# Performance work log

Measured on AMD Instinct MI355X. Metric: run time of the kernel, lower is better.

## Reference

```python
import jax, jax.numpy as jnp
import numpy as np

T, B, N, GH, GW, ENC, H, D, TH = 16, 512, 8192, 3, 13, 128, 4, 32, 64
G = GH * GW          # 39 social grid cells
EMB = H * D          # 128 = n_head * att_out
SCALE = 1.0 / np.sqrt(ENC).astype(np.float32)
LN_EPS = 1e-5


def lstm(x, Wih, Whh, bih, bhh):
    # x: [T, Batch, in] -> hidden states [T, Batch, ENC]; torch gate order i,f,g,o
    n = x.shape[1]
    h0 = jnp.zeros((n, ENC), x.dtype)

    def step(carry, xt):
        h, c = carry
        g = xt @ Wih.T + bih + h @ Whh.T + bhh
        i, f, gg, o = jnp.split(g, 4, axis=-1)
        c = jax.nn.sigmoid(f) * c + jax.nn.sigmoid(i) * jnp.tanh(gg)
        h = jax.nn.sigmoid(o) * jnp.tanh(c)
        return (h, c), h

    _, hs = jax.lax.scan(step, (h0, h0), x)
    return hs


def glu(x, Wa, ba, Wg, bg):
    return (x @ Wa.T + ba) * jax.nn.sigmoid(x @ Wg.T + bg)


def layer_norm(x, g, b):
    m = jnp.mean(x, -1, keepdims=True)
    v = jnp.var(x, -1, keepdims=True)
    return (x - m) * jax.lax.rsqrt(v + LN_EPS) * g + b


def setup_inputs():
    key = jax.random.key(0)
    ks = jax.random.split(key, 40)

    def rn(i, sh, s=1.0):
        return jax.random.normal(ks[i], sh, jnp.float32) * s

    inp = {
        'hist': rn(0, (T, B, 2)), 'nbrs': rn(1, (T, N, 2)),
        'va': rn(2, (T, B, 2)), 'nbrsva': rn(3, (T, N, 2)),
        'lane': jnp.zeros((T, B, 1), jnp.float32),
        'nbrslane': jnp.zeros((T, N, 1), jnp.float32),
        'cls': rn(4, (T, B, 1)), 'nbrscls': rn(5, (T, N, 1)),
    }
    # boolean social-grid mask with exactly N true cells (cell-level, full enc dim)
    rng = np.random.default_rng(0)
    flat = np.zeros(B * G, bool)
    flat[rng.permutation(B * G)[:N]] = True
    inp['mask'] = jnp.asarray(np.broadcast_to(flat.reshape(B, GH, GW, 1), (B, GH, GW, ENC)))

    s = 0.05
    inp.update({
        'W1': rn(6, (TH, 5), s), 'b1': jnp.zeros((TH,), jnp.float32),
        'Wih': rn(7, (4 * ENC, TH), s), 'Whh': rn(8, (4 * ENC, ENC), s),
        'bih': jnp.zeros((4 * ENC,), jnp.float32), 'bhh': jnp.zeros((4 * ENC,), jnp.float32),
        'Wq': rn(9, (EMB, ENC), s), 'bq': jnp.zeros((EMB,), jnp.float32),
        'Wk': rn(10, (EMB, ENC), s), 'bk': jnp.zeros((EMB,), jnp.float32),
        'Wv': rn(11, (EMB, ENC), s), 'bv': jnp.zeros((EMB,), jnp.float32),
        'Wg1a': rn(12, (ENC, EMB), s), 'bg1a': jnp.zeros((ENC,), jnp.float32),
        'Wg1g': rn(13, (ENC, EMB), s), 'bg1g': jnp.zeros((ENC,), jnp.float32),
        'Wqt': rn(14, (EMB, ENC), s), 'bqt': jnp.zeros((EMB,), jnp.float32),
        'Wkt': rn(15, (EMB, ENC), s), 'bkt': jnp.zeros((EMB,), jnp.float32),
        'Wvt': rn(16, (EMB, ENC), s), 'bvt': jnp.zeros((EMB,), jnp.float32),
        'Wg2a': rn(17, (ENC, EMB), s), 'bg2a': jnp.zeros((ENC,), jnp.float32),
        'Wg2g': rn(18, (ENC, EMB), s), 'bg2g': jnp.zeros((ENC,), jnp.float32),
        'ln_g': jnp.ones((ENC,), jnp.float32), 'ln_b': jnp.zeros((ENC,), jnp.float32),
    })
    return inp


def reference(hist, nbrs, mask, va, nbrsva, lane, nbrslane, cls, nbrscls,
              W1, b1, Wih, Whh, bih, bhh, Wq, bq, Wk, bk, Wv, bv,
              Wg1a, bg1a, Wg1g, bg1g, Wqt, bqt, Wkt, bkt, Wvt, bvt,
              Wg2a, bg2a, Wg2g, bg2g, ln_g, ln_b):
    # f_length == 5 branch
    hist_in = jnp.concatenate((hist, cls, va), -1)        # [T,B,5]
    nbrs_in = jnp.concatenate((nbrs, nbrscls, nbrsva), -1)  # [T,N,5]

    hist_enc = jax.nn.elu(hist_in @ W1.T + b1)
    hist_h = lstm(hist_enc, Wih, Whh, bih, bhh)           # [T,B,ENC]
    hist_hidden = jnp.transpose(hist_h, (1, 0, 2))        # [B,T,ENC]

    nbrs_enc = jax.nn.elu(nbrs_in @ W1.T + b1)
    nbrs_h = lstm(nbrs_enc, Wih, Whh, bih, bhh)           # [T,N,ENC]

    # masked_scatter: fill true grid cells (row-major over B*G) with neighbor states
    cell = mask[:, :, :, 0].reshape(B * G)                # [B*G] bool
    idx = jnp.cumsum(cell.astype(jnp.int32)) - 1          # position among true cells
    gathered = nbrs_h[:, jnp.clip(idx, 0, N - 1), :]      # [T,B*G,ENC]
    soc = jnp.where(cell[None, :, None], gathered, 0.0).reshape(T, B, G, ENC)

    # spatial multi-head attention (each timestep attends over its own grid)
    q = (hist_hidden @ Wq.T + bq).reshape(B, T, H, D)
    k = (soc @ Wk.T + bk).reshape(T, B, G, H, D)
    v = (soc @ Wv.T + bv).reshape(T, B, G, H, D)
    a = jax.nn.softmax(jnp.einsum('bthd,tbghd->bthg', q, k) * SCALE, -1)
    spa = jnp.einsum('bthg,tbghd->bthd', a, v).reshape(B, T, EMB)
    spa = glu(spa, Wg1a, bg1a, Wg1g, bg1g)

    values = layer_norm(hist_hidden + spa, ln_g, ln_b)    # [B,T,ENC]

    # temporal multi-head attention over T
    qt = (values @ Wqt.T + bqt).reshape(B, T, H, D)
    kt = (values @ Wkt.T + bkt).reshape(B, T, H, D)
    vt = (values @ Wvt.T + bvt).reshape(B, T, H, D)
    at = jax.nn.softmax(jnp.einsum('bthd,bshd->bhts', qt, kt) * SCALE, -1)
    tmp = jnp.einsum('bhts,bshd->bthd', at, vt).reshape(B, T, EMB)
    tmp = glu(tmp, Wg2a, bg2a, Wg2g, bg2g)

    # use_spatial=True
    return layer_norm(hist_hidden + spa + tmp, ln_g, ln_b)
```

## Files before the change

kernel.cpp:

```cpp
#include <hip/hip_runtime.h>
#include <math.h>

#define T_ 16
#define B_ 512
#define N_ 8192
#define G_ 39
#define ENC_ 128
#define TH_ 64
#define MROWS 8704
#define GATE 512
#define KCAT 192
#define SCALE_ 0.08838834764831845f
#define LNEPS 1e-5f
#define NBLK 136

typedef short bf16x8 __attribute__((ext_vector_type(8)));
typedef float f32x4  __attribute__((ext_vector_type(4)));

__device__ __forceinline__ float sigm(float x){ return 1.0f/(1.0f+expf(-x)); }
__device__ __forceinline__ float rcpf(float x){ return __builtin_amdgcn_rcpf(x); }
__device__ __forceinline__ float sigm_f(float x){ return rcpf(1.0f + __expf(-x)); }
__device__ __forceinline__ float tanh_f(float x){ return 1.0f - 2.0f*rcpf(__expf(2.0f*x) + 1.0f); }
__device__ __forceinline__ unsigned short f2bf(float f){
  unsigned int u = __float_as_uint(f);
  unsigned int r = u + 0x7FFFu + ((u>>16)&1u);
  return (unsigned short)(r>>16);
}
__device__ __forceinline__ float bf2f(unsigned short h){
  return __uint_as_float(((unsigned int)h)<<16);
}

__global__ __launch_bounds__(256) void k_prep(
    const float* __restrict__ Wih, const float* __restrict__ Whh,
    const float* __restrict__ bih, const float* __restrict__ bhh,
    const float* __restrict__ Wk,  const float* __restrict__ Wv,
    const float* __restrict__ Wq,
    const float* __restrict__ Wqt, const float* __restrict__ bqt,
    const float* __restrict__ Wkt, const float* __restrict__ bkt,
    const float* __restrict__ Wvt, const float* __restrict__ bvt,
    const float* __restrict__ Wg1a, const float* __restrict__ bg1a,
    const float* __restrict__ Wg1g, const float* __restrict__ bg1g,
    const float* __restrict__ Wg2a, const float* __restrict__ bg2a,
    const float* __restrict__ Wg2g, const float* __restrict__ bg2g,
    unsigned short* __restrict__ WcatB, float* __restrict__ biasg,
    unsigned short* __restrict__ WqB,
    unsigned short* __restrict__ WkD,  unsigned short* __restrict__ WvD,
    float* __restrict__ zero512,
    unsigned short* __restrict__ WqktB, float* __restrict__ bqkt,
    unsigned short* __restrict__ Wg1B,  float* __restrict__ bg1,
    unsigned short* __restrict__ Wg2B,  float* __restrict__ bg2)
{
  int i = blockIdx.x*256 + threadIdx.x;
  if (i < GATE*KCAT) {
    int n = i / KCAT, k = i % KCAT;
    WcatB[i] = f2bf((k < TH_) ? Wih[n*TH_ + k] : Whh[n*ENC_ + (k - TH_)]);
  }
  if (i < GATE) biasg[i] = bih[i] + bhh[i];
  if (i < ENC_*ENC_) WqB[i] = f2bf(Wq[i]);
  if (i < 512*128) {
    int r = i >> 7, dc = i & 127;
    int h = r >> 7, e = r & 127;
    WkD[i] = ((dc >> 5) == h) ? f2bf(Wk[dc*128 + e]) : (unsigned short)0;
  }
  if (i < 128*512) {
    int r = i >> 9, kk = i & 511;
    int hp = kk >> 7, e = kk & 127;
    WvD[i] = (hp == (r >> 5)) ? f2bf(Wv[r*128 + e]) : (unsigned short)0;
  }
  if (i < 512) zero512[i] = 0.0f;
  if (i < 2*ENC_*ENC_) {
    int n = i >> 7, k = i & 127;
    Wg1B[i] = f2bf((n < ENC_) ? Wg1a[n*ENC_ + k] : Wg1g[(n-ENC_)*ENC_ + k]);
    Wg2B[i] = f2bf((n < ENC_) ? Wg2a[n*ENC_ + k] : Wg2g[(n-ENC_)*ENC_ + k]);
  }
  if (i < 2*ENC_) {
    bg1[i] = (i < ENC_) ? bg1a[i] : bg1g[i-ENC_];
    bg2[i] = (i < ENC_) ? bg2a[i] : bg2g[i-ENC_];
  }
  if (i < 3*ENC_*ENC_) {
    int n = i >> 7, k = i & 127;
    float w = (n < ENC_) ? Wqt[n*ENC_ + k] : (n < 2*ENC_) ? Wkt[(n-ENC_)*ENC_ + k]
                                                          : Wvt[(n-2*ENC_)*ENC_ + k];
    WqktB[i] = f2bf(w);
  }
  if (i < 3*ENC_) bqkt[i] = (i < ENC_) ? bqt[i] : (i < 2*ENC_) ? bkt[i-ENC_] : bvt[i-2*ENC_];
}

__device__ __forceinline__ int cellval(const unsigned char* m, long cell, int w) {
  long byte = cell * 128L * w;
  if (w == 1) return m[byte] != 0;
  if (w == 2) return *(const unsigned short*)(m + byte) != 0;
  if (w == 4) return *(const unsigned int*)(m + byte) != 0;
  return *(const unsigned long long*)(m + byte) != 0ULL;
}
__device__ __forceinline__ int cellconsist(const unsigned char* m, long cell, int w) {
  long byte = cell * 128L * w;
  if (w == 1) { unsigned char v = m[byte];
    for (int j = 1; j < 8; ++j) if (m[byte + j] != v) return 0; return 1; }
  if (w == 2) { unsigned short v = *(const unsigned short*)(m + byte);
    for (int j = 1; j < 8; ++j) if (*(const unsigned short*)(m + byte + 2L*j) != v) return 0; return 1; }
  if (w == 4) { unsigned int v = *(const unsigned int*)(m + byte);
    for (int j = 1; j < 8; ++j) if (*(const unsigned int*)(m + byte + 4L*j) != v) return 0; return 1; }
  unsigned long long v = *(const unsigned long long*)(m + byte);
  for (int j = 1; j < 8; ++j) if (*(const unsigned long long*)(m + byte + 8L*j) != v) return 0; return 1;
}

__global__ void k_detect(const unsigned char* __restrict__ mask, int* __restrict__ wsel)
{
  __shared__ int bad;
  int tid = threadIdx.x;
  int chosen = 0;
  for (int w = 1; w <= 8 && !chosen; w <<= 1) {
    if (tid == 0) bad = 0;
    __syncthreads();
    int ok = 1;
    for (int c = tid; c < 512; c += 256) ok &= cellconsist(mask, c, w);
    if (!ok) bad = 1;
    __syncthreads();
    if (!bad) chosen = w;
    __syncthreads();
  }
  if (tid == 0) *wsel = chosen ? chosen : 1;
}

__global__ void k_count(const unsigned char* __restrict__ mask,
                        const int* __restrict__ wsel, int* __restrict__ bcnt)
{
  __shared__ int sc[256];
  int tid = threadIdx.x;
  long cell = (long)blockIdx.x*256 + tid;
  sc[tid] = cellval(mask, cell, *wsel);
  __syncthreads();
  for (int off = 128; off; off >>= 1) {
    if (tid < off) sc[tid] += sc[tid + off];
    __syncthreads();
  }
  if (tid == 0) bcnt[blockIdx.x] = sc[0];
}

__global__ void k_fill(const unsigned char* __restrict__ mask,
                       const int* __restrict__ wsel, const int* __restrict__ bcnt,
                       int* __restrict__ nidx)
{
  __shared__ int sc[256];
  int tid = threadIdx.x, blk = blockIdx.x;
  long cell = (long)blk*256 + tid;
  int on = cellval(mask, cell, *wsel);
  sc[tid] = on;
  __syncthreads();
  for (int off = 1; off < 256; off <<= 1) {
    int v = (tid >= off) ? sc[tid - off] : 0;
    __syncthreads();
    sc[tid] += v;
    __syncthreads();
  }
  int base = 0;
  for (int i = 0; i < blk; ++i) base += bcnt[i];
  nidx[cell] = on ? (base + sc[tid] - 1) : -1;
}

__global__ __launch_bounds__(256) void k_encode_all(
    const float* __restrict__ hist, const float* __restrict__ cls, const float* __restrict__ va,
    const float* __restrict__ nbrs, const float* __restrict__ nbrscls, const float* __restrict__ nbrsva,
    const float* __restrict__ W1, const float* __restrict__ b1,
    unsigned short* __restrict__ XencB)
{
  int i = blockIdx.x*256 + threadIdx.x;
  int t = blockIdx.y;
  int o = i & 63, m = i >> 6;
  float in0, in1, in2, in3, in4;
  if (m < B_) {
    int r = t*B_ + m;
    in0 = hist[r*2]; in1 = hist[r*2+1]; in2 = cls[r]; in3 = va[r*2]; in4 = va[r*2+1];
  } else {
    int r = t*N_ + (m - B_);
    in0 = nbrs[r*2]; in1 = nbrs[r*2+1]; in2 = nbrscls[r]; in3 = nbrsva[r*2]; in4 = nbrsva[r*2+1];
  }
  const float* w = W1 + o*5;
  float s = b1[o] + in0*w[0] + in1*w[1] + in2*w[2] + in3*w[3] + in4*w[4];
  XencB[((long)t*MROWS + m)*64 + o] = f2bf((s > 0.0f) ? s : expm1f(s));
}

struct AP {
  const unsigned short *Xenc, *Wcat, *Wq;
  const float *biasg, *bq;
  float *hh;
  unsigned short *qB;
  unsigned short *HnB;
};

__global__ __launch_bounds__(512, 1) void k_lstm(AP p)
{
  __shared__ unsigned short Hl[2*64*128];

  const int tid = threadIdx.x;
  const int w = tid >> 6, l = tid & 63;
  const int lr = l & 15, lk = (l >> 4) * 8, lq = (l >> 4) * 4;
  const int bi = blockIdx.x, bm = bi * 64;
  const bool ish = (bi < 8);

  bf16x8 wgx[4][2], wgh[4][4];
  #pragma unroll
  for (int g = 0; g < 4; ++g) {
    #pragma unroll
    for (int ks = 0; ks < 2; ++ks)
      wgx[g][ks] = *(const bf16x8*)(p.Wcat + (long)(g*128 + w*16 + lr)*KCAT + ks*32 + lk);
    #pragma unroll
    for (int ks = 0; ks < 4; ++ks)
      wgh[g][ks] = *(const bf16x8*)(p.Wcat + (long)(g*128 + w*16 + lr)*KCAT + 64 + ks*32 + lk);
  }

  const int ch = w*16 + lr;
  float bgv[4];
  #pragma unroll
  for (int g = 0; g < 4; ++g) bgv[g] = p.biasg[g*128 + ch];
  const float bqv = ish ? p.bq[ch] : 0.0f;

  for (int i = tid; i < 64*128; i += 512) Hl[i] = 0;
  float creg[4][4];
  #pragma unroll
  for (int mi = 0; mi < 4; ++mi)
    #pragma unroll
    for (int q = 0; q < 4; ++q) creg[mi][q] = 0.0f;

  bf16x8 axc[2][4];
  #pragma unroll
  for (int ks = 0; ks < 2; ++ks)
    #pragma unroll
    for (int mi = 0; mi < 4; ++mi)
      axc[ks][mi] = *(const bf16x8*)(p.Xenc + ((long)0*MROWS + bm + mi*16 + lr)*64 + ks*32 + lk);

  __syncthreads();

  int cur = 0;
  for (int t = 0; t < T_; ++t) {
    f32x4 acc[4][4];
    #pragma unroll
    for (int g = 0; g < 4; ++g)
      #pragma unroll
      for (int mi = 0; mi < 4; ++mi) {
        f32x4 v = { bgv[g], bgv[g], bgv[g], bgv[g] };
        acc[g][mi] = v;
      }
    #pragma unroll
    for (int ks = 0; ks < 2; ++ks)
      #pragma unroll
      for (int g = 0; g < 4; ++g)
        #pragma unroll
        for (int mi = 0; mi < 4; ++mi)
          acc[g][mi] = __builtin_amdgcn_mfma_f32_16x16x32_bf16(axc[ks][mi], wgx[g][ks], acc[g][mi], 0, 0, 0);
    if (t + 1 < T_) {
      #pragma unroll
      for (int ks = 0; ks < 2; ++ks)
        #pragma unroll
        for (int mi = 0; mi < 4; ++mi)
          axc[ks][mi] = *(const bf16x8*)(p.Xenc + ((long)(t+1)*MROWS + bm + mi*16 + lr)*64 + ks*32 + lk);
    }
    #pragma unroll
    for (int ks = 0; ks < 4; ++ks) {
      bf16x8 a[4];
      #pragma unroll
      for (int mi = 0; mi < 4; ++mi) {
        int row = mi*16 + lr;
        int col = (ks*32 + lk) ^ ((row & 7) << 3);
        a[mi] = *(const bf16x8*)(Hl + cur*8192 + row*128 + col);
      }
      #pragma unroll
      for (int g = 0; g < 4; ++g)
        #pragma unroll
        for (int mi = 0; mi < 4; ++mi)
          acc[g][mi] = __builtin_amdgcn_mfma_f32_16x16x32_bf16(a[mi], wgh[g][ks], acc[g][mi], 0, 0, 0);
    }
    int nxt = cur ^ 1;
    #pragma unroll
    for (int mi = 0; mi < 4; ++mi)
      #pragma unroll
      for (int q = 0; q < 4; ++q) {
        int row = mi*16 + lq + q;
        float gi = acc[0][mi][q];
        float gf = acc[1][mi][q];
        float gg = acc[2][mi][q];
        float go = acc[3][mi][q];
        float cc = sigm_f(gf)*creg[mi][q] + sigm_f(gi)*tanh_f(gg);
        creg[mi][q] = cc;
        float hv = sigm_f(go)*tanh_f(cc);
        Hl[nxt*8192 + row*128 + (ch ^ ((row & 7) << 3))] = f2bf(hv);
        if (ish) p.hh[((long)(bm + row)*T_ + t)*128 + ch] = hv;
      }
    __builtin_amdgcn_sched_barrier(0);
    asm volatile("s_waitcnt lgkmcnt(0)" ::: "memory");
    __builtin_amdgcn_s_barrier();
    __builtin_amdgcn_sched_barrier(0);
    cur = nxt;
    if (ish) {
      f32x4 a2[4];
      #pragma unroll
      for (int mi = 0; mi < 4; ++mi) {
        f32x4 v = { bqv, bqv, bqv, bqv };
        a2[mi] = v;
      }
      #pragma unroll
      for (int ks = 0; ks < 4; ++ks) {
        bf16x8 b = *(const bf16x8*)(p.Wq + (long)(w*16 + lr)*128 + ks*32 + lk);
        #pragma unroll
        for (int mi = 0; mi < 4; ++mi) {
          int row = mi*16 + lr;
          int col = (ks*32 + lk) ^ ((row & 7) << 3);
          bf16x8 a = *(const bf16x8*)(Hl + cur*8192 + row*128 + col);
          a2[mi] = __builtin_amdgcn_mfma_f32_16x16x32_bf16(a, b, a2[mi], 0, 0, 0);
        }
      }
      #pragma unroll
      for (int mi = 0; mi < 4; ++mi)
        #pragma unroll
        for (int q = 0; q < 4; ++q)
          p.qB[((long)t*B_ + bm + mi*16 + lq + q)*128 + ch] = f2bf(a2[mi][q]);
    } else {
      for (int e = tid; e < 64*16; e += 512) {
        int r = e >> 4, j = e & 15;
        int src = cur*8192 + r*128 + ((j*8) ^ ((r & 7) << 3));
        *(bf16x8*)(p.HnB + ((long)t*N_ + (bm - B_) + r)*128 + j*8) =
            *(const bf16x8*)(Hl + src);
      }
    }
  }
}

__global__ __launch_bounds__(128) void k_attn2(
    const unsigned short* __restrict__ qB,
    const unsigned short* __restrict__ qWB,
    const unsigned short* __restrict__ HnB,
    const float* __restrict__ bk,
    const int* __restrict__ nidx,
    unsigned short* __restrict__ hbarB)
{
  __shared__ int sn[G_];
  __shared__ unsigned short hL[G_*128];
  __shared__ float sgh[G_][4];
  int blk = blockIdx.x;
  int b = blk >> 4, t = blk & 15;
  int tid = threadIdx.x;
  int h = tid >> 5, d = tid & 31;
  if (tid < G_) sn[tid] = nidx[b*G_ + tid];
  __syncthreads();
  for (int g = 0; g < G_; ++g) {
    int ni = sn[g];
    if (ni >= 0) hL[g*128 + tid] = HnB[((long)t*N_ + ni)*128 + tid];
  }
  float qel = bf2f(qB[((long)t*B_ + b)*128 + tid]);
  float qbk = qel * bk[tid];
  #pragma unroll
  for (int off = 16; off; off >>= 1) qbk += __shfl_xor(qbk, off);
  float qw[4];
  #pragma unroll
  for (int j = 0; j < 4; ++j)
    qw[j] = bf2f(qWB[((long)t*B_ + b)*512 + h*128 + d + j*32]);
  __syncthreads();
  for (int g = 0; g < G_; ++g) {
    float s;
    if (sn[g] >= 0) {
      float part = 0.0f;
      #pragma unroll
      for (int j = 0; j < 4; ++j) part += bf2f(hL[g*128 + d + j*32]) * qw[j];
      #pragma unroll
      for (int off = 16; off; off >>= 1) part += __shfl_xor(part, off);
      s = (part + qbk) * SCALE_;
    } else {
      s = qbk * SCALE_;
    }
    if (d == 0) sgh[g][h] = s;
  }
  float mx = -1e30f;
  for (int g = 0; g < G_; ++g) mx = fmaxf(mx, sgh[g][h]);
  float den = 0.0f;
  float hb[4] = {0.0f, 0.0f, 0.0f, 0.0f};
  for (int g = 0; g < G_; ++g) {
    float e = expf(sgh[g][h] - mx);
    den += e;
    if (sn[g] >= 0) {
      #pragma unroll
      for (int j = 0; j < 4; ++j) hb[j] += e * bf2f(hL[g*128 + d + j*32]);
    }
  }
  float inv = 1.0f / den;
  #pragma unroll
  for (int j = 0; j < 4; ++j)
    hbarB[((long)b*T_ + t)*512 + h*128 + d + j*32] = f2bf(hb[j] * inv);
}

__global__ __launch_bounds__(256) void k_gemm_bf16(
    const unsigned short* __restrict__ A, int lda,
    const unsigned short* __restrict__ W, int ldw,
    const float* __restrict__ bias,
    float* __restrict__ C, int ldc, int K)
{
  int tid = threadIdx.x;
  int w = tid >> 6, l = tid & 63;
  int lr = l & 15, lk = (l >> 4) * 8, lq = (l >> 4) * 4;
  int bm = blockIdx.x * 64;
  int bn = blockIdx.y * 128 + w * 32;
  f32x4 acc[4][2] = {};
  for (int k0 = 0; k0 < K; k0 += 32) {
    bf16x8 a[4], b[2];
    #pragma unroll
    for (int mi = 0; mi < 4; ++mi)
      a[mi] = *(const bf16x8*)(A + (long)(bm + mi*16 + lr)*lda + k0 + lk);
    #pragma unroll
    for (int ni = 0; ni < 2; ++ni)
      b[ni] = *(const bf16x8*)(W + (long)(bn + ni*16 + lr)*ldw + k0 + lk);
    #pragma unroll
    for (int mi = 0; mi < 4; ++mi)
      #pragma unroll
      for (int ni = 0; ni < 2; ++ni)
        acc[mi][ni] = __builtin_amdgcn_mfma_f32_16x16x32_bf16(a[mi], b[ni], acc[mi][ni], 0, 0, 0);
  }
  #pragma unroll
  for (int mi = 0; mi < 4; ++mi)
    #pragma unroll
    for (int ni = 0; ni < 2; ++ni) {
      int col = bn + ni*16 + lr;
      float bb = bias[col];
      #pragma unroll
      for (int q = 0; q < 4; ++q)
        C[(long)(bm + mi*16 + lq + q)*ldc + col] = acc[mi][ni][q] + bb;
    }
}

__global__ __launch_bounds__(256) void k_gemm_bf16o(
    const unsigned short* __restrict__ A, int lda,
    const unsigned short* __restrict__ W, int ldw,
    const float* __restrict__ bias,
    unsigned short* __restrict__ C, int ldc, int K)
{
  int tid = threadIdx.x;
  int w = tid >> 6, l = tid & 63;
  int lr = l & 15, lk = (l >> 4) * 8, lq = (l >> 4) * 4;
  int bm = blockIdx.x * 64;
  int bn = blockIdx.y * 128 + w * 32;
  f32x4 acc[4][2] = {};
  for (int k0 = 0; k0 < K; k0 += 32) {
    bf16x8 a[4], b[2];
    #pragma unroll
    for (int mi = 0; mi < 4; ++mi)
      a[mi] = *(const bf16x8*)(A + (long)(bm + mi*16 + lr)*lda + k0 + lk);
    #pragma unroll
    for (int ni = 0; ni < 2; ++ni)
      b[ni] = *(const bf16x8*)(W + (long)(bn + ni*16 + lr)*ldw + k0 + lk);
    #pragma unroll
    for (int mi = 0; mi < 4; ++mi)
      #pragma unroll
      for (int ni = 0; ni < 2; ++ni)
        acc[mi][ni] = __builtin_amdgcn_mfma_f32_16x16x32_bf16(a[mi], b[ni], acc[mi][ni], 0, 0, 0);
  }
  #pragma unroll
  for (int mi = 0; mi < 4; ++mi)
    #pragma unroll
    for (int ni = 0; ni < 2; ++ni) {
      int col = bn + ni*16 + lr;
      float bb = bias[col];
      #pragma unroll
      for (int q = 0; q < 4; ++q)
        C[(long)(bm + mi*16 + lq + q)*ldc + col] = f2bf(acc[mi][ni][q] + bb);
    }
}

__global__ __launch_bounds__(256) void k_glu_addln(
    const float* __restrict__ t12, const float* __restrict__ res,
    const float* __restrict__ lg, const float* __restrict__ lb,
    float* __restrict__ sum_out, unsigned short* __restrict__ ln_bf16,
    float* __restrict__ ln_f32)
{
  int gtid = blockIdx.x*256 + threadIdx.x;
  int r = gtid >> 6;
  int l = threadIdx.x & 63;
  if (r >= B_*T_) return;
  long b4 = (long)r*256, b2 = (long)r*128;
  float xA = res[b2 + l]      + t12[b4 + l]      * sigm(t12[b4 + 128 + l]);
  float xB = res[b2 + 64 + l] + t12[b4 + 64 + l] * sigm(t12[b4 + 192 + l]);
  if (sum_out) { sum_out[b2 + l] = xA; sum_out[b2 + 64 + l] = xB; }
  float s = xA + xB, s2 = xA*xA + xB*xB;
  #pragma unroll
  for (int off = 32; off; off >>= 1) { s += __shfl_xor(s, off); s2 += __shfl_xor(s2, off); }
  float mean = s * (1.0f/128.0f);
  float var  = s2 * (1.0f/128.0f) - mean*mean;
  float inv  = rsqrtf(var + LNEPS);
  float oA = (xA - mean)*inv*lg[l]      + lb[l];
  float oB = (xB - mean)*inv*lg[64 + l] + lb[64 + l];
  if (ln_bf16) { ln_bf16[b2 + l] = f2bf(oA); ln_bf16[b2 + 64 + l] = f2bf(oB); }
  if (ln_f32)  { ln_f32[b2 + l] = oA;        ln_f32[b2 + 64 + l] = oB; }
}

__global__ __launch_bounds__(128) void k_attn_t(
    const unsigned short* __restrict__ qkt, unsigned short* __restrict__ out)
{
  int b = blockIdx.x, tid = threadIdx.x;
  __shared__ float sq[16][128], sk[16][128], sv[16][128];
  __shared__ float sc[16][4][16];
  for (int i = tid; i < T_*ENC_; i += 128) {
    int tt = i >> 7, j = i & 127;
    long a = ((long)b*T_ + tt)*384;
    sq[tt][j] = bf2f(qkt[a + j]);
    sk[tt][j] = bf2f(qkt[a + 128 + j]);
    sv[tt][j] = bf2f(qkt[a + 256 + j]);
  }
  __syncthreads();
  for (int e = tid; e < 1024; e += 128) {
    int t = e >> 6, s = (e >> 2) & 15, h2 = e & 3;
    float pp = 0.0f;
    #pragma unroll
    for (int d2 = 0; d2 < 32; ++d2) pp += sq[t][h2*32 + d2] * sk[s][h2*32 + d2];
    sc[t][h2][s] = pp * SCALE_;
  }
  __syncthreads();
  if (tid < 64) {
    int t = tid >> 2, h2 = tid & 3;
    float mx = -1e30f;
    for (int s = 0; s < 16; ++s) mx = fmaxf(mx, sc[t][h2][s]);
    float sum = 0.0f;
    for (int s = 0; s < 16; ++s) { float e2 = expf(sc[t][h2][s] - mx); sc[t][h2][s] = e2; sum += e2; }
    float inv = 1.0f / sum;
    for (int s = 0; s < 16; ++s) sc[t][h2][s] *= inv;
  }
  __syncthreads();
  int h2 = tid >> 5, d2 = tid & 31;
  for (int t = 0; t < 16; ++t) {
    float acc = 0.0f;
    for (int s = 0; s < 16; ++s) acc += sc[t][h2][s] * sv[s][h2*32 + d2];
    out[((long)b*T_ + t)*128 + tid] = f2bf(acc);
  }
}

extern "C" void kernel_launch(void* const* d_in, const int* in_sizes, int n_in,
                              void* d_out, int out_size, void* d_ws, size_t ws_size,
                              hipStream_t stream)
{
  const float* hist    = (const float*)d_in[0];
  const float* nbrs    = (const float*)d_in[1];
  const float* va      = (const float*)d_in[2];
  const float* nbrsva  = (const float*)d_in[3];
  const float* cls     = (const float*)d_in[6];
  const float* nbrscls = (const float*)d_in[7];
  const unsigned char* mask = (const unsigned char*)d_in[8];
  const float* W1  = (const float*)d_in[9];
  const float* b1  = (const float*)d_in[10];
  const float* Wih = (const float*)d_in[11];
  const float* Whh = (const float*)d_in[12];
  const float* bih = (const float*)d_in[13];
  const float* bhh = (const float*)d_in[14];
  const float* Wq  = (const float*)d_in[15];
  const float* bq  = (const float*)d_in[16];
  const float* Wk  = (const float*)d_in[17];
  const float* bk  = (const float*)d_in[18];
  const float* Wv  = (const float*)d_in[19];
  const float* bv  = (const float*)d_in[20];
  const float* Wg1a = (const float*)d_in[21];
  const float* bg1a = (const float*)d_in[22];
  const float* Wg1g = (const float*)d_in[23];
  const float* bg1g = (const float*)d_in[24];
  const float* Wqt = (const float*)d_in[25];
  const float* bqt = (const float*)d_in[26];
  const float* Wkt = (const float*)d_in[27];
  const float* bkt = (const float*)d_in[28];
  const float* Wvt = (const float*)d_in[29];
  const float* bvt = (const float*)d_in[30];
  const float* Wg2a = (const float*)d_in[31];
  const float* bg2a = (const float*)d_in[32];
  const float* Wg2g = (const float*)d_in[33];
  const float* bg2g = (const float*)d_in[34];
  const float* ln_g = (const float*)d_in[35];
  const float* ln_b = (const float*)d_in[36];

  char* base = (char*)d_ws;
  size_t off = 0;
  auto alloc = [&](size_t bytes) { char* r = base + off; off = (off + bytes + 255) & ~(size_t)255; return r; };
  unsigned short* WcatB = (unsigned short*)alloc(GATE*KCAT*2);
  float*          biasg = (float*)alloc(GATE*4);
  unsigned short* WqB   = (unsigned short*)alloc(ENC_*ENC_*2);
  unsigned short* WkD   = (unsigned short*)alloc(512*128*2);
  unsigned short* WvD   = (unsigned short*)alloc(128*512*2);
  float*          zero512 = (float*)alloc(512*4);
  unsigned short* WqktB = (unsigned short*)alloc(3*ENC_*ENC_*2);
  float*          bqkt  = (float*)alloc(3*ENC_*4);
  unsigned short* Wg1B  = (unsigned short*)alloc(2*ENC_*ENC_*2);
  float*          bg1   = (float*)alloc(2*ENC_*4);
  unsigned short* Wg2B  = (unsigned short*)alloc(2*ENC_*ENC_*2);
  float*          bg2   = (float*)alloc(2*ENC_*4);
  unsigned short* XencB = (unsigned short*)alloc((size_t)T_*MROWS*64*2);
  float*          hh    = (float*)alloc((size_t)B_*T_*ENC_*4);
  unsigned short* qB    = (unsigned short*)alloc((size_t)T_*B_*ENC_*2);
  unsigned short* HnB   = (unsigned short*)alloc((size_t)T_*N_*ENC_*2);
  unsigned short* qWB   = (unsigned short*)alloc((size_t)T_*B_*512*2);
  unsigned short* hbarB = (unsigned short*)alloc((size_t)B_*T_*512*2);
  unsigned short* spaB  = (unsigned short*)alloc((size_t)B_*T_*ENC_*2);
  float*          t12   = (float*)alloc((size_t)B_*T_*2*ENC_*4);
  float*          S1    = (float*)alloc((size_t)B_*T_*ENC_*4);
  unsigned short* valsB = (unsigned short*)alloc((size_t)B_*T_*ENC_*2);
  unsigned short* qktB  = (unsigned short*)alloc((size_t)B_*T_*3*ENC_*2);
  unsigned short* atoB  = (unsigned short*)alloc((size_t)B_*T_*ENC_*2);
  int*            nidx  = (int*)alloc((size_t)B_*G_*4);
  int*            bcnt  = (int*)alloc(78*4);
  int*            wsel  = (int*)alloc(4);

  const int ROWS = B_*T_;

  k_prep<<<384, 256, 0, stream>>>(
      Wih, Whh, bih, bhh, Wk, Wv, Wq,
      Wqt, bqt, Wkt, bkt, Wvt, bvt,
      Wg1a, bg1a, Wg1g, bg1g, Wg2a, bg2a, Wg2g, bg2g,
      WcatB, biasg, WqB, WkD, WvD, zero512, WqktB, bqkt, Wg1B, bg1, Wg2B, bg2);
  k_detect<<<1, 256, 0, stream>>>(mask, wsel);
  k_count<<<78, 256, 0, stream>>>(mask, wsel, bcnt);
  k_fill<<<78, 256, 0, stream>>>(mask, wsel, bcnt, nidx);
  k_encode_all<<<dim3(MROWS*64/256, T_), 256, 0, stream>>>(
      hist, cls, va, nbrs, nbrscls, nbrsva, W1, b1, XencB);

  AP ap;
  ap.Xenc = XencB; ap.Wcat = WcatB; ap.Wq = WqB;
  ap.biasg = biasg; ap.bq = bq;
  ap.hh = hh; ap.qB = qB; ap.HnB = HnB;
  k_lstm<<<NBLK, 512, 0, stream>>>(ap);

  k_gemm_bf16o<<<dim3(ROWS/64, 4), 256, 0, stream>>>(qB, 128, WkD, 128, zero512, qWB, 512, 128);
  k_attn2<<<ROWS, 128, 0, stream>>>(qB, qWB, HnB, bk, nidx, hbarB);
  k_gemm_bf16o<<<dim3(ROWS/64, 1), 256, 0, stream>>>(hbarB, 512, WvD, 512, bv, spaB, 128, 512);

  k_gemm_bf16<<<dim3(ROWS/64, 2), 256, 0, stream>>>(spaB, 128, Wg1B, 128, bg1, t12, 256, 128);
  k_glu_addln<<<(ROWS*64)/256, 256, 0, stream>>>(t12, hh, ln_g, ln_b, S1, valsB, nullptr);
  k_gemm_bf16o<<<dim3(ROWS/64, 3), 256, 0, stream>>>(valsB, 128, WqktB, 128, bqkt, qktB, 384, 128);
  k_attn_t<<<B_, 128, 0, stream>>>(qktB, atoB);
  k_gemm_bf16<<<dim3(ROWS/64, 2), 256, 0, stream>>>(atoB, 128, Wg2B, 128, bg2, t12, 256, 128);
  k_glu_addln<<<(ROWS*64)/256, 256, 0, stream>>>(t12, S1, ln_g, ln_b, nullptr, nullptr, (float*)d_out);
}
```

Baseline: 366.8 us.

## Split LSTM block across 16 waves and stream gate weights from global memory

The LSTM kernel now runs 1024 threads per block: 16 waves arranged as 2 row groups by 8 column groups, each owning 32 rows instead of 64. Gate weights are no longer kept in registers. They are reloaded from global memory (cache) at every timestep, and the next-step Xenc prefetch is removed. This doubles wave-level parallelism on the serial recurrence and reduces register pressure. In exchange it adds repeated weight loads on the critical path and more barrier participants.

```diff
diff --git a/kernel.cpp b/kernel.cpp
--- a/kernel.cpp
+++ b/kernel.cpp
@@ -189,94 +189,78 @@
   unsigned short *HnB;
 };
 
-__global__ __launch_bounds__(512, 1) void k_lstm(AP p)
+__global__ __launch_bounds__(1024, 1) void k_lstm(AP p)
 {
   __shared__ unsigned short Hl[2*64*128];
 
   const int tid = threadIdx.x;
   const int w = tid >> 6, l = tid & 63;
   const int lr = l & 15, lk = (l >> 4) * 8, lq = (l >> 4) * 4;
+  const int rg = w >> 3, cg = w & 7;
   const int bi = blockIdx.x, bm = bi * 64;
   const bool ish = (bi < 8);
 
-  bf16x8 wgx[4][2], wgh[4][4];
-  #pragma unroll
-  for (int g = 0; g < 4; ++g) {
-    #pragma unroll
-    for (int ks = 0; ks < 2; ++ks)
-      wgx[g][ks] = *(const bf16x8*)(p.Wcat + (long)(g*128 + w*16 + lr)*KCAT + ks*32 + lk);
-    #pragma unroll
-    for (int ks = 0; ks < 4; ++ks)
-      wgh[g][ks] = *(const bf16x8*)(p.Wcat + (long)(g*128 + w*16 + lr)*KCAT + 64 + ks*32 + lk);
-  }
-
-  const int ch = w*16 + lr;
+  const int ch = cg*16 + lr;
   float bgv[4];
   #pragma unroll
   for (int g = 0; g < 4; ++g) bgv[g] = p.biasg[g*128 + ch];
   const float bqv = ish ? p.bq[ch] : 0.0f;
 
-  for (int i = tid; i < 64*128; i += 512) Hl[i] = 0;
-  float creg[4][4];
-  #pragma unroll
-  for (int mi = 0; mi < 4; ++mi)
+  for (int i = tid; i < 64*128; i += 1024) Hl[i] = 0;
+  float creg[2][4];
+  #pragma unroll
+  for (int mi = 0; mi < 2; ++mi)
     #pragma unroll
     for (int q = 0; q < 4; ++q) creg[mi][q] = 0.0f;
-
-  bf16x8 axc[2][4];
-  #pragma unroll
-  for (int ks = 0; ks < 2; ++ks)
-    #pragma unroll
-    for (int mi = 0; mi < 4; ++mi)
-      axc[ks][mi] = *(const bf16x8*)(p.Xenc + ((long)0*MROWS + bm + mi*16 + lr)*64 + ks*32 + lk);
-
   __syncthreads();
 
   int cur = 0;
   for (int t = 0; t < T_; ++t) {
-    f32x4 acc[4][4];
+    f32x4 acc[4][2];
     #pragma unroll
     for (int g = 0; g < 4; ++g)
       #pragma unroll
-      for (int mi = 0; mi < 4; ++mi) {
+      for (int mi = 0; mi < 2; ++mi) {
         f32x4 v = { bgv[g], bgv[g], bgv[g], bgv[g] };
         acc[g][mi] = v;
       }
     #pragma unroll
-    for (int ks = 0; ks < 2; ++ks)
-      #pragma unroll
-      for (int g = 0; g < 4; ++g)
+    for (int ks = 0; ks < 2; ++ks) {
+      bf16x8 a[2];
+      #pragma unroll
+      for (int mi = 0; mi < 2; ++mi)
+        a[mi] = *(const bf16x8*)(p.Xenc + ((long)t*MROWS + bm + rg*32 + mi*16 + lr)*64 + ks*32 + lk);
+      #pragma unroll
+      for (int g = 0; g < 4; ++g) {
+        bf16x8 b = *(const bf16x8*)(p.Wcat + (long)(g*128 + ch)*KCAT + ks*32 + lk);
         #pragma unroll
-        for (int mi = 0; mi < 4; ++mi)
-          acc[g][mi] = __builtin_amdgcn_mfma_f32_16x16x32_bf16(axc[ks][mi], wgx[g][ks], acc[g][mi], 0, 0, 0);
-    if (t + 1 < T_) {
-      #pragma unroll
-      for (int ks = 0; ks < 2; ++ks)
-        #pragma unroll
-        for (int mi = 0; mi < 4; ++mi)
-          axc[ks][mi] = *(const bf16x8*)(p.Xenc + ((long)(t+1)*MROWS + bm + mi*16 + lr)*64 + ks*32 + lk);
+        for (int mi = 0; mi < 2; ++mi)
+          acc[g][mi] = __builtin_amdgcn_mfma_f32_16x16x32_bf16(a[mi], b, acc[g][mi], 0, 0, 0);
+      }
     }
     #pragma unroll
     for (int ks = 0; ks < 4; ++ks) {
-      bf16x8 a[4];
-      #pragma unroll
-      for (int mi = 0; mi < 4; ++mi) {
-        int row = mi*16 + lr;
+      bf16x8 a[2];
+      #pragma unroll
+      for (int mi = 0; mi < 2; ++mi) {
+        int row = rg*32 + mi*16 + lr;
         int col = (ks*32 + lk) ^ ((row & 7) << 3);
         a[mi] = *(const bf16x8*)(Hl + cur*8192 + row*128 + col);
       }
       #pragma unroll
-      for (int g = 0; g < 4; ++g)
+      for (int g = 0; g < 4; ++g) {
+        bf16x8 b = *(const bf16x8*)(p.Wcat + (long)(g*128 + ch)*KCAT + 64 + ks*32 + lk);
         #pragma unroll
-        for (int mi = 0; mi < 4; ++mi)
-          acc[g][mi] = __builtin_amdgcn_mfma_f32_16x16x32_bf16(a[mi], wgh[g][ks], acc[g][mi], 0, 0, 0);
+        for (int mi = 0; mi < 2; ++mi)
+          acc[g][mi] = __builtin_amdgcn_mfma_f32_16x16x32_bf16(a[mi], b, acc[g][mi], 0, 0, 0);
+      }
     }
     int nxt = cur ^ 1;
     #pragma unroll
-    for (int mi = 0; mi < 4; ++mi)
+    for (int mi = 0; mi < 2; ++mi)
       #pragma unroll
       for (int q = 0; q < 4; ++q) {
-        int row = mi*16 + lq + q;
+        int row = rg*32 + mi*16 + lq + q;
         float gi = acc[0][mi][q];
         float gf = acc[1][mi][q];
         float gg = acc[2][mi][q];
@@ -293,35 +277,33 @@
     __builtin_amdgcn_sched_barrier(0);
     cur = nxt;
     if (ish) {
-      f32x4 a2[4];
-      #pragma unroll
-      for (int mi = 0; mi < 4; ++mi) {
+      f32x4 a2[2];
+      #pragma unroll
+      for (int mi = 0; mi < 2; ++mi) {
         f32x4 v = { bqv, bqv, bqv, bqv };
         a2[mi] = v;
       }
       #pragma unroll
       for (int ks = 0; ks < 4; ++ks) {
-        bf16x8 b = *(const bf16x8*)(p.Wq + (long)(w*16 + lr)*128 + ks*32 + lk);
+        bf16x8 b = *(const bf16x8*)(p.Wq + (long)ch*128 + ks*32 + lk);
         #pragma unroll
-        for (int mi = 0; mi < 4; ++mi) {
-          int row = mi*16 + lr;
+        for (int mi = 0; mi < 2; ++mi) {
+          int row = rg*32 + mi*16 + lr;
           int col = (ks*32 + lk) ^ ((row & 7) << 3);
           bf16x8 a = *(const bf16x8*)(Hl + cur*8192 + row*128 + col);
           a2[mi] = __builtin_amdgcn_mfma_f32_16x16x32_bf16(a, b, a2[mi], 0, 0, 0);
         }
       }
       #pragma unroll
-      for (int mi = 0; mi < 4; ++mi)
+      for (int mi = 0; mi < 2; ++mi)
         #pragma unroll
         for (int q = 0; q < 4; ++q)
-          p.qB[((long)t*B_ + bm + mi*16 + lq + q)*128 + ch] = f2bf(a2[mi][q]);
+          p.qB[((long)t*B_ + bm + rg*32 + mi*16 + lq + q)*128 + ch] = f2bf(a2[mi][q]);
     } else {
-      for (int e = tid; e < 64*16; e += 512) {
-        int r = e >> 4, j = e & 15;
-        int src = cur*8192 + r*128 + ((j*8) ^ ((r & 7) << 3));
-        *(bf16x8*)(p.HnB + ((long)t*N_ + (bm - B_) + r)*128 + j*8) =
-            *(const bf16x8*)(Hl + src);
-      }
+      int r = tid >> 4, j = tid & 15;
+      int src = cur*8192 + r*128 + ((j*8) ^ ((r & 7) << 3));
+      *(bf16x8*)(p.HnB + ((long)t*N_ + (bm - B_) + r)*128 + j*8) =
+          *(const bf16x8*)(Hl + src);
     }
   }
 }
@@ -618,7 +600,7 @@
   ap.Xenc = XencB; ap.Wcat = WcatB; ap.Wq = WqB;
   ap.biasg = biasg; ap.bq = bq;
   ap.hh = hh; ap.qB = qB; ap.HnB = HnB;
-  k_lstm<<<NBLK, 512, 0, stream>>>(ap);
+  k_lstm<<<NBLK, 1024, 0, stream>>>(ap);
 
   k_gemm_bf16o<<<dim3(ROWS/64, 4), 256, 0, stream>>>(qB, 128, WkD, 128, zero512, qWB, 512, 128);
   k_attn2<<<ROWS, 128, 0, stream>>>(qB, qWB, HnB, bk, nidx, hbarB);
```

Measured after the change: 458.6 us. 25.1% more time.
